# Kernel tuning notes

Hardware: AMD Instinct MI355X
Metric: run time of the kernel (lower is better)

## Reference

```python
import jax, jax.numpy as jnp
import numpy as np


def setup_inputs() -> dict:
    key = jax.random.key(0)
    ks = jax.random.split(key, 8)
    C, R = 256, 16
    Cqk = C // R  # 16
    B, H, W = 8, 64, 64
    x = jax.random.normal(ks[0], (B, C, H, W), dtype=jnp.float32)
    # 1x1 conv weights stored as [out, in] (kernel dims squeezed)
    s = 1.0 / np.sqrt(C)
    Wq = jax.random.uniform(ks[1], (Cqk, C), minval=-s, maxval=s, dtype=jnp.float32)
    bq = jax.random.uniform(ks[2], (Cqk,), minval=-s, maxval=s, dtype=jnp.float32)
    Wk = jax.random.uniform(ks[3], (Cqk, C), minval=-s, maxval=s, dtype=jnp.float32)
    bk = jax.random.uniform(ks[4], (Cqk,), minval=-s, maxval=s, dtype=jnp.float32)
    Wv = jax.random.uniform(ks[5], (C, C), minval=-s, maxval=s, dtype=jnp.float32)
    bv = jax.random.uniform(ks[6], (C,), minval=-s, maxval=s, dtype=jnp.float32)
    gamma = jnp.float32(0.1)  # nonzero so the attention branch affects output
    return {"x": x, "Wq": Wq, "bq": bq, "Wk": Wk, "bk": bk, "Wv": Wv, "bv": bv, "gamma": gamma}


def reference(x, Wq, bq, Wk, bk, Wv, bv, gamma):
    B, C, H, W = x.shape
    N = H * W
    xf = x.reshape(B, C, N)  # [B, C, N]
    # 1x1 convs == per-pixel linear over channel dim
    q = jnp.einsum('oc,bcn->bon', Wq, xf) + bq[None, :, None]  # [B, Cqk, N]
    k = jnp.einsum('oc,bcn->bon', Wk, xf) + bk[None, :, None]  # [B, Cqk, N]
    v = jnp.einsum('oc,bcn->bon', Wv, xf) + bv[None, :, None]  # [B, C, N]
    # scores[b, i, j] = q[:, i] . k[:, j]; no scale factor (faithful to source)
    scores = jnp.einsum('bdn,bdm->bnm', q, k)  # [B, N, N]
    attn = jax.nn.softmax(scores, axis=-1)
    # y[b, c, i] = sum_j v[b, c, j] * attn[b, i, j]
    y = jnp.einsum('bcm,bnm->bcn', v, attn).reshape(B, C, H, W)
    return x + gamma * y
```

## Files before the change

kernel.cpp:

```cpp
#include <hip/hip_runtime.h>
#include <hip/hip_bf16.h>
#include <math.h>

typedef short bf16x8 __attribute__((ext_vector_type(8)));
typedef float f32x4 __attribute__((ext_vector_type(4)));

#define MFMA_B16(A, B, C) __builtin_amdgcn_mfma_f32_16x16x32_bf16(A, B, C, 0, 0, 0)

#define NBATCH 8
#define CIN 256
#define NPIX 4096
#define L2E 1.4426950408889634f
#define THR2 8.0f

__device__ __forceinline__ unsigned short f2b(float f) {
    union { float f; unsigned int u; } v;
    v.f = f;
    return (unsigned short)((v.u + 0x7fffu + ((v.u >> 16) & 1u)) >> 16);
}

__device__ __forceinline__ unsigned int cvtpk(float lo, float hi) {
    unsigned int r;
    asm volatile("v_cvt_pk_bf16_f32 %0, %1, %2" : "=v"(r) : "v"(lo), "v"(hi));
    return r;
}

__global__ void packw_kernel(const float* __restrict__ Wq, const float* __restrict__ Wk,
                             const float* __restrict__ Wv,
                             unsigned short* __restrict__ wv_bf,
                             unsigned short* __restrict__ wqk_bf) {
    int t = blockIdx.x * 256 + threadIdx.x;
    if (t < 65536) {
        wv_bf[t] = f2b(Wv[t]);
    } else {
        int u = t - 65536;
        int r = u >> 8, c = u & 255;
        float v = (r < 16) ? Wq[r * 256 + c] * L2E : Wk[(r - 16) * 256 + c];
        wqk_bf[u] = f2b(v);
    }
}

__global__ __launch_bounds__(256, 2) void qkv_kernel(
    const float* __restrict__ x,
    const unsigned short* __restrict__ wv_bf, const unsigned short* __restrict__ wqk_bf,
    const float* __restrict__ bq, const float* __restrict__ bk, const float* __restrict__ bv,
    unsigned short* __restrict__ qT, unsigned short* __restrict__ kT,
    unsigned short* __restrict__ vv)
{
    constexpr int XSTR = 264;
    __shared__ __align__(16) unsigned short xs[64 * XSTR];
    const int b     = blockIdx.x >> 6;
    const int nbase = (blockIdx.x & 63) * 64;
    const int tid = threadIdx.x;
    const int w  = tid >> 6;
    const int l  = tid & 63;
    const int g  = l >> 4;
    const int ln = l & 15;

    {
        const float* xp = x + (size_t)b * CIN * NPIX + nbase + l;
        unsigned short* xsp = xs + l * XSTR + w * 64;
        #pragma unroll
        for (int cc = 0; cc < 32; ++cc) {
            float v0 = xp[(size_t)(w * 64 + 2 * cc)     * NPIX];
            float v1 = xp[(size_t)(w * 64 + 2 * cc + 1) * NPIX];
            unsigned int pk = (unsigned int)f2b(v0) | ((unsigned int)f2b(v1) << 16);
            *(unsigned int*)(xsp + 2 * cc) = pk;
        }
    }
    __syncthreads();

    const f32x4 vzero = {0.f, 0.f, 0.f, 0.f};
    f32x4 acc[4][4];
    f32x4 accq[4];
    #pragma unroll
    for (int i = 0; i < 4; ++i) {
        accq[i] = vzero;
        #pragma unroll
        for (int j = 0; j < 4; ++j) acc[i][j] = vzero;
    }

    for (int ks = 0; ks < 8; ++ks) {
        const int k0 = ks * 32;
        bf16x8 xf[4];
        #pragma unroll
        for (int nt = 0; nt < 4; ++nt)
            xf[nt] = *(const bf16x8*)(xs + (nt * 16 + ln) * XSTR + k0 + g * 8);
        #pragma unroll
        for (int ct = 0; ct < 4; ++ct) {
            const bf16x8 wf = *(const bf16x8*)(wv_bf + (size_t)(w * 64 + ct * 16 + ln) * CIN + k0 + g * 8);
            #pragma unroll
            for (int nt = 0; nt < 4; ++nt)
                acc[ct][nt] = MFMA_B16(wf, xf[nt], acc[ct][nt]);
        }
        if (w < 2) {
            const bf16x8 wfq = *(const bf16x8*)(wqk_bf + (size_t)(w * 16 + ln) * CIN + k0 + g * 8);
            #pragma unroll
            for (int nt = 0; nt < 4; ++nt)
                accq[nt] = MFMA_B16(wfq, xf[nt], accq[nt]);
        }
    }

    #pragma unroll
    for (int ct = 0; ct < 4; ++ct) {
        #pragma unroll
        for (int r = 0; r < 4; ++r) {
            const int c = w * 64 + ct * 16 + g * 4 + r;
            const float bias = bv[c];
            #pragma unroll
            for (int nt = 0; nt < 4; ++nt)
                vv[((size_t)b * CIN + c) * NPIX + nbase + nt * 16 + ln] =
                    f2b(acc[ct][nt][r] + bias);
        }
    }
    if (w < 2) {
        unsigned short* oq = (w == 0 ? qT : kT);
        #pragma unroll
        for (int r = 0; r < 4; ++r) {
            const int d = g * 4 + r;
            const float bi = (w == 0 ? bq[d] * L2E : bk[d]);
            #pragma unroll
            for (int nt = 0; nt < 4; ++nt)
                oq[((size_t)b * NPIX + nbase + nt * 16 + ln) * 32 + d] =
                    f2b(accq[nt][r] + bi);
        }
    } else {
        unsigned short* oq = (w == 2 ? qT : kT);
        unsigned short* p  = oq + ((size_t)b * NPIX + nbase + l) * 32 + 16;
        uint4 z; z.x = 0; z.y = 0; z.z = 0; z.w = 0;
        *(uint4*)p       = z;
        *(uint4*)(p + 8) = z;
    }
}

__global__ __launch_bounds__(256, 2) void attn_kernel(
    const float* __restrict__ x, const float* __restrict__ gamma_p,
    const unsigned short* __restrict__ qT, const unsigned short* __restrict__ kT,
    const unsigned short* __restrict__ vv, float* __restrict__ out)
{
    const int b     = blockIdx.x & 7;
    const int qbase = (blockIdx.x >> 3) * 64;
    const int tid = threadIdx.x;
    const int wid = tid >> 6;
    const int wq  = wid & 1;
    const int wc  = wid >> 1;
    const int l   = tid & 63;
    const int ln  = l & 15;
    const int g   = l >> 4;
    const float gamma = *gamma_p;

    const int srcA = ln + ((g & 1) << 5);
    const int srcB = srcA + 16;
    const bool hi  = (g >> 1) != 0;

    bf16x8 qf[2];
    #pragma unroll
    for (int qt = 0; qt < 2; ++qt)
        qf[qt] = *(const bf16x8*)(qT + ((size_t)b * NPIX + qbase + wq * 32 + qt * 16 + ln) * 32 + g * 8);

    const f32x4 vzero = {0.f, 0.f, 0.f, 0.f};
    f32x4 acc[2][8];
    #pragma unroll
    for (int i = 0; i < 2; ++i)
        #pragma unroll
        for (int j = 0; j < 8; ++j) acc[i][j] = vzero;
    float m_run[2]  = {-INFINITY, -INFINITY};
    float l_part[2] = {0.f, 0.f};

    const unsigned short* kbase = kT + (size_t)b * NPIX * 32;
    const unsigned short* vbase = vv + ((size_t)b * CIN + wc * 128) * NPIX;

    for (int kt = 0; kt < 64; ++kt) {
        const int k0 = kt * 64;
        bf16x8 kf[4];
        #pragma unroll
        for (int ws = 0; ws < 4; ++ws)
            kf[ws] = *(const bf16x8*)(kbase + (size_t)(k0 + 16 * ws + ln) * 32 + g * 8);

        f32x4 s[2][4];
        #pragma unroll
        for (int qt = 0; qt < 2; ++qt)
            #pragma unroll
            for (int ws = 0; ws < 4; ++ws)
                s[qt][ws] = MFMA_B16(kf[ws], qf[qt], vzero);

        unsigned int pk[2][4][2];
        #pragma unroll
        for (int qt = 0; qt < 2; ++qt) {
            float pml = fmaxf(fmaxf(s[qt][0][0], s[qt][0][1]), fmaxf(s[qt][0][2], s[qt][0][3]));
            #pragma unroll
            for (int ws = 1; ws < 4; ++ws)
                pml = fmaxf(pml, fmaxf(fmaxf(s[qt][ws][0], s[qt][ws][1]),
                                       fmaxf(s[qt][ws][2], s[qt][ws][3])));
            if (__any(pml > m_run[qt] + THR2)) {
                float pm = fmaxf(pml, __shfl_xor(pml, 16));
                pm = fmaxf(pm, __shfl_xor(pm, 32));
                float mn = fmaxf(m_run[qt], pm);
                float sc = exp2f(m_run[qt] - mn);
                #pragma unroll
                for (int ct = 0; ct < 8; ++ct) acc[qt][ct] *= sc;
                l_part[qt] *= sc;
                m_run[qt] = mn;
            }
            float ts = 0.f;
            #pragma unroll
            for (int ws = 0; ws < 4; ++ws)
                #pragma unroll
                for (int r = 0; r < 4; ++r) {
                    float p = exp2f(s[qt][ws][r] - m_run[qt]);
                    s[qt][ws][r] = p;
                    ts += p;
                }
            l_part[qt] += ts;
            #pragma unroll
            for (int ws = 0; ws < 4; ++ws) {
                pk[qt][ws][0] = cvtpk(s[qt][ws][0], s[qt][ws][1]);
                pk[qt][ws][1] = cvtpk(s[qt][ws][2], s[qt][ws][3]);
            }
        }

        #pragma unroll
        for (int kk = 0; kk < 2; ++kk) {
            bf16x8 pf[2];
            #pragma unroll
            for (int qt = 0; qt < 2; ++qt) {
                unsigned int aL0 = __shfl((int)pk[qt][2 * kk][0],     srcA);
                unsigned int aL1 = __shfl((int)pk[qt][2 * kk][1],     srcA);
                unsigned int aH0 = __shfl((int)pk[qt][2 * kk + 1][0], srcA);
                unsigned int aH1 = __shfl((int)pk[qt][2 * kk + 1][1], srcA);
                unsigned int bL0 = __shfl((int)pk[qt][2 * kk][0],     srcB);
                unsigned int bL1 = __shfl((int)pk[qt][2 * kk][1],     srcB);
                unsigned int bH0 = __shfl((int)pk[qt][2 * kk + 1][0], srcB);
                unsigned int bH1 = __shfl((int)pk[qt][2 * kk + 1][1], srcB);
                union { unsigned int u[4]; bf16x8 v; } pu;
                pu.u[0] = hi ? aH0 : aL0;
                pu.u[1] = hi ? aH1 : aL1;
                pu.u[2] = hi ? bH0 : bL0;
                pu.u[3] = hi ? bH1 : bL1;
                pf[qt] = pu.v;
            }
            __builtin_amdgcn_s_setprio(1);
            #pragma unroll
            for (int ct = 0; ct < 8; ++ct) {
                const bf16x8 vf = *(const bf16x8*)(
                    vbase + (size_t)(ct * 16 + ln) * NPIX + k0 + kk * 32 + g * 8);
                acc[0][ct] = MFMA_B16(vf, pf[0], acc[0][ct]);
                acc[1][ct] = MFMA_B16(vf, pf[1], acc[1][ct]);
            }
            __builtin_amdgcn_s_setprio(0);
        }
    }

    #pragma unroll
    for (int qt = 0; qt < 2; ++qt) {
        float lt = l_part[qt];
        lt += __shfl_xor(lt, 16);
        lt += __shfl_xor(lt, 32);
        const float inv = 1.0f / lt;
        const int n = qbase + wq * 32 + qt * 16 + ln;
        #pragma unroll
        for (int ct = 0; ct < 8; ++ct) {
            #pragma unroll
            for (int r = 0; r < 4; ++r) {
                const int c = wc * 128 + ct * 16 + g * 4 + r;
                const size_t idx = ((size_t)b * CIN + c) * NPIX + n;
                out[idx] = x[idx] + gamma * (acc[qt][ct][r] * inv);
            }
        }
    }
}

extern "C" void kernel_launch(void* const* d_in, const int* in_sizes, int n_in,
                              void* d_out, int out_size, void* d_ws, size_t ws_size,
                              hipStream_t stream) {
    const float* x     = (const float*)d_in[0];
    const float* Wq    = (const float*)d_in[1];
    const float* bq    = (const float*)d_in[2];
    const float* Wk    = (const float*)d_in[3];
    const float* bk    = (const float*)d_in[4];
    const float* Wv    = (const float*)d_in[5];
    const float* bv    = (const float*)d_in[6];
    const float* gamma = (const float*)d_in[7];

    unsigned short* qTp  = (unsigned short*)d_ws;
    unsigned short* kTp  = qTp + (size_t)NBATCH * NPIX * 32;
    unsigned short* vvp  = kTp + (size_t)NBATCH * NPIX * 32;
    unsigned short* wvb  = vvp + (size_t)NBATCH * CIN * NPIX;
    unsigned short* wqkb = wvb + 256 * 256;

    packw_kernel<<<288, 256, 0, stream>>>(Wq, Wk, Wv, wvb, wqkb);
    qkv_kernel<<<512, 256, 0, stream>>>(x, wvb, wqkb, bq, bk, bv, qTp, kTp, vvp);
    attn_kernel<<<512, 256, 0, stream>>>(x, gamma, qTp, kTp, vvp, (float*)d_out);
}
```

Measured before the change: 371.9 us.

## Give each attention wave one query tile and double waves per block

Each wave now processes a single 16-query tile instead of two, and the block grows to 8 waves (512 threads) with launch bounds targeting 4 blocks per CU. This halves accumulator and softmax state registers per wave to raise occupancy and latency hiding. In exchange, every V and K fragment loaded from global memory feeds half as many MFMAs, roughly doubling load traffic per unit of compute.

```diff
diff --git a/kernel.cpp b/kernel.cpp
--- a/kernel.cpp
+++ b/kernel.cpp
@@ -133,7 +133,7 @@
     }
 }
 
-__global__ __launch_bounds__(256, 2) void attn_kernel(
+__global__ __launch_bounds__(512, 4) void attn_kernel(
     const float* __restrict__ x, const float* __restrict__ gamma_p,
     const unsigned short* __restrict__ qT, const unsigned short* __restrict__ kT,
     const unsigned short* __restrict__ vv, float* __restrict__ out)
@@ -142,8 +142,8 @@
     const int qbase = (blockIdx.x >> 3) * 64;
     const int tid = threadIdx.x;
     const int wid = tid >> 6;
-    const int wq  = wid & 1;
-    const int wc  = wid >> 1;
+    const int wq  = wid & 3;
+    const int wc  = wid >> 2;
     const int l   = tid & 63;
     const int ln  = l & 15;
     const int g   = l >> 4;
@@ -153,19 +153,14 @@
     const int srcB = srcA + 16;
     const bool hi  = (g >> 1) != 0;
 
-    bf16x8 qf[2];
-    #pragma unroll
-    for (int qt = 0; qt < 2; ++qt)
-        qf[qt] = *(const bf16x8*)(qT + ((size_t)b * NPIX + qbase + wq * 32 + qt * 16 + ln) * 32 + g * 8);
+    const bf16x8 qf = *(const bf16x8*)(qT + ((size_t)b * NPIX + qbase + wq * 16 + ln) * 32 + g * 8);
 
     const f32x4 vzero = {0.f, 0.f, 0.f, 0.f};
-    f32x4 acc[2][8];
-    #pragma unroll
-    for (int i = 0; i < 2; ++i)
-        #pragma unroll
-        for (int j = 0; j < 8; ++j) acc[i][j] = vzero;
-    float m_run[2]  = {-INFINITY, -INFINITY};
-    float l_part[2] = {0.f, 0.f};
+    f32x4 acc[8];
+    #pragma unroll
+    for (int j = 0; j < 8; ++j) acc[j] = vzero;
+    float m_run  = -INFINITY;
+    float l_part = 0.f;
 
     const unsigned short* kbase = kT + (size_t)b * NPIX * 32;
     const unsigned short* vbase = vv + ((size_t)b * CIN + wc * 128) * NPIX;
@@ -177,95 +172,82 @@
         for (int ws = 0; ws < 4; ++ws)
             kf[ws] = *(const bf16x8*)(kbase + (size_t)(k0 + 16 * ws + ln) * 32 + g * 8);
 
-        f32x4 s[2][4];
-        #pragma unroll
-        for (int qt = 0; qt < 2; ++qt)
-            #pragma unroll
-            for (int ws = 0; ws < 4; ++ws)
-                s[qt][ws] = MFMA_B16(kf[ws], qf[qt], vzero);
-
-        unsigned int pk[2][4][2];
-        #pragma unroll
-        for (int qt = 0; qt < 2; ++qt) {
-            float pml = fmaxf(fmaxf(s[qt][0][0], s[qt][0][1]), fmaxf(s[qt][0][2], s[qt][0][3]));
-            #pragma unroll
-            for (int ws = 1; ws < 4; ++ws)
-                pml = fmaxf(pml, fmaxf(fmaxf(s[qt][ws][0], s[qt][ws][1]),
-                                       fmaxf(s[qt][ws][2], s[qt][ws][3])));
-            if (__any(pml > m_run[qt] + THR2)) {
-                float pm = fmaxf(pml, __shfl_xor(pml, 16));
-                pm = fmaxf(pm, __shfl_xor(pm, 32));
-                float mn = fmaxf(m_run[qt], pm);
-                float sc = exp2f(m_run[qt] - mn);
-                #pragma unroll
-                for (int ct = 0; ct < 8; ++ct) acc[qt][ct] *= sc;
-                l_part[qt] *= sc;
-                m_run[qt] = mn;
+        f32x4 s[4];
+        #pragma unroll
+        for (int ws = 0; ws < 4; ++ws)
+            s[ws] = MFMA_B16(kf[ws], qf, vzero);
+
+        float pml = fmaxf(fmaxf(s[0][0], s[0][1]), fmaxf(s[0][2], s[0][3]));
+        #pragma unroll
+        for (int ws = 1; ws < 4; ++ws)
+            pml = fmaxf(pml, fmaxf(fmaxf(s[ws][0], s[ws][1]), fmaxf(s[ws][2], s[ws][3])));
+        if (__any(pml > m_run + THR2)) {
+            float pm = fmaxf(pml, __shfl_xor(pml, 16));
+            pm = fmaxf(pm, __shfl_xor(pm, 32));
+            float mn = fmaxf(m_run, pm);
+            float sc = exp2f(m_run - mn);
+            #pragma unroll
+            for (int ct = 0; ct < 8; ++ct) acc[ct] *= sc;
+            l_part *= sc;
+            m_run = mn;
+        }
+        float ts = 0.f;
+        #pragma unroll
+        for (int ws = 0; ws < 4; ++ws)
+            #pragma unroll
+            for (int r = 0; r < 4; ++r) {
+                float p = exp2f(s[ws][r] - m_run);
+                s[ws][r] = p;
+                ts += p;
             }
-            float ts = 0.f;
-            #pragma unroll
-            for (int ws = 0; ws < 4; ++ws)
-                #pragma unroll
-                for (int r = 0; r < 4; ++r) {
-                    float p = exp2f(s[qt][ws][r] - m_run[qt]);
-                    s[qt][ws][r] = p;
-                    ts += p;
-                }
-            l_part[qt] += ts;
-            #pragma unroll
-            for (int ws = 0; ws < 4; ++ws) {
-                pk[qt][ws][0] = cvtpk(s[qt][ws][0], s[qt][ws][1]);
-                pk[qt][ws][1] = cvtpk(s[qt][ws][2], s[qt][ws][3]);
-            }
+        l_part += ts;
+        unsigned int pk[4][2];
+        #pragma unroll
+        for (int ws = 0; ws < 4; ++ws) {
+            pk[ws][0] = cvtpk(s[ws][0], s[ws][1]);
+            pk[ws][1] = cvtpk(s[ws][2], s[ws][3]);
         }
 
         #pragma unroll
         for (int kk = 0; kk < 2; ++kk) {
-            bf16x8 pf[2];
-            #pragma unroll
-            for (int qt = 0; qt < 2; ++qt) {
-                unsigned int aL0 = __shfl((int)pk[qt][2 * kk][0],     srcA);
-                unsigned int aL1 = __shfl((int)pk[qt][2 * kk][1],     srcA);
-                unsigned int aH0 = __shfl((int)pk[qt][2 * kk + 1][0], srcA);
-                unsigned int aH1 = __shfl((int)pk[qt][2 * kk + 1][1], srcA);
-                unsigned int bL0 = __shfl((int)pk[qt][2 * kk][0],     srcB);
-                unsigned int bL1 = __shfl((int)pk[qt][2 * kk][1],     srcB);
-                unsigned int bH0 = __shfl((int)pk[qt][2 * kk + 1][0], srcB);
-                unsigned int bH1 = __shfl((int)pk[qt][2 * kk + 1][1], srcB);
-                union { unsigned int u[4]; bf16x8 v; } pu;
-                pu.u[0] = hi ? aH0 : aL0;
-                pu.u[1] = hi ? aH1 : aL1;
-                pu.u[2] = hi ? bH0 : bL0;
-                pu.u[3] = hi ? bH1 : bL1;
-                pf[qt] = pu.v;
-            }
+            unsigned int aL0 = __shfl((int)pk[2 * kk][0],     srcA);
+            unsigned int aL1 = __shfl((int)pk[2 * kk][1],     srcA);
+            unsigned int aH0 = __shfl((int)pk[2 * kk + 1][0], srcA);
+            unsigned int aH1 = __shfl((int)pk[2 * kk + 1][1], srcA);
+            unsigned int bL0 = __shfl((int)pk[2 * kk][0],     srcB);
+            unsigned int bL1 = __shfl((int)pk[2 * kk][1],     srcB);
+            unsigned int bH0 = __shfl((int)pk[2 * kk + 1][0], srcB);
+            unsigned int bH1 = __shfl((int)pk[2 * kk + 1][1], srcB);
+            union { unsigned int u[4]; bf16x8 v; } pu;
+            pu.u[0] = hi ? aH0 : aL0;
+            pu.u[1] = hi ? aH1 : aL1;
+            pu.u[2] = hi ? bH0 : bL0;
+            pu.u[3] = hi ? bH1 : bL1;
+            const bf16x8 pf = pu.v;
+
             __builtin_amdgcn_s_setprio(1);
             #pragma unroll
             for (int ct = 0; ct < 8; ++ct) {
                 const bf16x8 vf = *(const bf16x8*)(
                     vbase + (size_t)(ct * 16 + ln) * NPIX + k0 + kk * 32 + g * 8);
-                acc[0][ct] = MFMA_B16(vf, pf[0], acc[0][ct]);
-                acc[1][ct] = MFMA_B16(vf, pf[1], acc[1][ct]);
+                acc[ct] = MFMA_B16(vf, pf, acc[ct]);
             }
             __builtin_amdgcn_s_setprio(0);
         }
     }
 
-    #pragma unroll
-    for (int qt = 0; qt < 2; ++qt) {
-        float lt = l_part[qt];
-        lt += __shfl_xor(lt, 16);
-        lt += __shfl_xor(lt, 32);
-        const float inv = 1.0f / lt;
-        const int n = qbase + wq * 32 + qt * 16 + ln;
-        #pragma unroll
-        for (int ct = 0; ct < 8; ++ct) {
-            #pragma unroll
-            for (int r = 0; r < 4; ++r) {
-                const int c = wc * 128 + ct * 16 + g * 4 + r;
-                const size_t idx = ((size_t)b * CIN + c) * NPIX + n;
-                out[idx] = x[idx] + gamma * (acc[qt][ct][r] * inv);
-            }
+    float lt = l_part;
+    lt += __shfl_xor(lt, 16);
+    lt += __shfl_xor(lt, 32);
+    const float inv = 1.0f / lt;
+    const int n = qbase + wq * 16 + ln;
+    #pragma unroll
+    for (int ct = 0; ct < 8; ++ct) {
+        #pragma unroll
+        for (int r = 0; r < 4; ++r) {
+            const int c = wc * 128 + ct * 16 + g * 4 + r;
+            const size_t idx = ((size_t)b * CIN + c) * NPIX + n;
+            out[idx] = x[idx] + gamma * (acc[ct][r] * inv);
         }
     }
 }
@@ -290,5 +272,5 @@
 
     packw_kernel<<<288, 256, 0, stream>>>(Wq, Wk, Wv, wvb, wqkb);
     qkv_kernel<<<512, 256, 0, stream>>>(x, wvb, wqkb, bq, bk, bv, qTp, kTp, vvp);
-    attn_kernel<<<512, 256, 0, stream>>>(x, gamma, qTp, kTp, vvp, (float*)d_out);
-}
+    attn_kernel<<<512, 512, 0, stream>>>(x, gamma, qTp, kTp, vvp, (float*)d_out);
+}
```

Measured after the change: 617.1 us. +65.9%, slower.
